# Optimization experiments

Hardware: AMD Instinct MI355X
Metric: run time of the kernel (lower is better)

## Reference

```python
import jax, jax.numpy as jnp
import numpy as np

D = 4096
N_HEAD = 32
KV_HEAD = 8
GS = D * KV_HEAD // N_HEAD  # 1024, kv projection width
B, S = 1, 2048


def setup_inputs() -> dict:
    key = jax.random.key(0)
    ks = jax.random.split(key, 10)
    sc = 0.02
    return {
        "x": jax.random.normal(ks[0], (B, S, D), dtype=jnp.float32),
        "y": jax.random.normal(ks[1], (B, S, D), dtype=jnp.float32),
        "Wq": jax.random.normal(ks[2], (D, D), dtype=jnp.float32) * sc,
        "bq": jax.random.normal(ks[3], (D,), dtype=jnp.float32) * sc,
        "Wk": jax.random.normal(ks[4], (D, GS), dtype=jnp.float32) * sc,
        "bk": jax.random.normal(ks[5], (GS,), dtype=jnp.float32) * sc,
        "Wv": jax.random.normal(ks[6], (D, GS), dtype=jnp.float32) * sc,
        "bv": jax.random.normal(ks[7], (GS,), dtype=jnp.float32) * sc,
        "Wo": jax.random.normal(ks[8], (D, D), dtype=jnp.float32) * sc,
        "bo": jax.random.normal(ks[9], (D,), dtype=jnp.float32) * sc,
        "n_head": N_HEAD,
        "kv_head": KV_HEAD,
    }


def reference(x, y, Wq, bq, Wk, bk, Wv, bv, Wo, bo, n_head, kv_head):
    b, s, d = x.shape
    hd = d // n_head              # per-head dim
    gvs = hd // 2                 # complex pairs per head (group_vector_size)
    q = (x @ Wq + bq).reshape(b, s, n_head, hd)
    k = (y @ Wk + bk).reshape(b, s, kv_head, hd)
    v = (y @ Wv + bv).reshape(b, s, kv_head, hd)

    # RoPE: phi = 1/5000**(i/gvs); angle[p, i] = phi[i] * p  (matrix.T in torch)
    phi = 1.0 / (5000.0 ** (jnp.arange(gvs, dtype=jnp.float32) / gvs))
    ang = jnp.arange(s, dtype=jnp.float32)[:, None] * phi[None, :]  # [S, gvs]
    cos = jnp.cos(ang)[None, :, None, :]  # [1,S,1,gvs]
    sin = jnp.sin(ang)[None, :, None, :]

    def rope(t):
        # interleaved pairs (t[...,2i], t[...,2i+1]) form complex numbers
        tr, ti = t[..., 0::2], t[..., 1::2]
        ro = tr * cos - ti * sin
        io = tr * sin + ti * cos
        return jnp.stack([ro, io], axis=-1).reshape(t.shape)

    q = rope(q)
    k = rope(k)

    # GQA: head h uses kv head h // (n_head // kv_head) -> repeat kv heads
    module = n_head // kv_head
    k = jnp.repeat(k, module, axis=2)  # [B,S,H,hd]
    v = jnp.repeat(v, module, axis=2)

    scores = jnp.einsum("bqhd,bkhd->bhqk", q, k) / jnp.sqrt(jnp.float32(hd))
    causal = jnp.tril(jnp.ones((s, s), dtype=bool))
    scores = jnp.where(causal[None, None], scores, -jnp.inf)
    attn = jax.nn.softmax(scores, axis=-1)
    out = jnp.einsum("bhqk,bkhd->bqhd", attn, v).reshape(b, s, d)
    return out @ Wo + bo
```

## Files before the change

### kernel.cpp

```cpp
#include <hip/hip_runtime.h>
#include <hip/hip_bf16.h>

typedef unsigned int uint32;
typedef unsigned short ushort16;
typedef __attribute__((ext_vector_type(8))) __bf16 bf16x8;
typedef __attribute__((ext_vector_type(4))) float f32x4;

__device__ __forceinline__ ushort16 f2bf(float f) {
    uint32 u = __float_as_uint(f);
    u += 0x7fff + ((u >> 16) & 1);
    return (ushort16)(u >> 16);
}
__device__ __forceinline__ uint32 pack2rn(float a, float b) {
    uint32 ua = __float_as_uint(a) + 0x8000u;
    uint32 ub = __float_as_uint(b) + 0x8000u;
    return __builtin_amdgcn_perm(ub, ua, 0x07060302);
}
__device__ __forceinline__ float blo(uint32 u) { return __uint_as_float(u << 16); }
__device__ __forceinline__ float bhi(uint32 u) { return __uint_as_float(u & 0xffff0000u); }

__device__ __forceinline__ void storeC(float v, float* p) { *p = v; }
__device__ __forceinline__ void storeC(float v, ushort16* p) { *p = f2bf(v); }

template <typename OutT>
__global__ __launch_bounds__(256) void gemm_mfma(
    const float* __restrict__ A, const float* __restrict__ W1,
    const float* __restrict__ W2, int ldw,
    const float* __restrict__ b1, const float* __restrict__ b2,
    OutT* __restrict__ C, int N, int K, int nsplit)
{
    __shared__ ushort16 As[128 * 64];
    __shared__ ushort16 Bs[128 * 64];

    const int tid  = threadIdx.x;
    const int lane = tid & 63, wave = tid >> 6;
    const int quad = lane >> 4, m16 = lane & 15;
    const int wm = (wave >> 1) * 64, wn = (wave & 1) * 64;
    const int gm0 = blockIdx.y * 128, gn0 = blockIdx.x * 128;

    const float* Wuse = (gn0 < nsplit) ? W1 : W2;
    const int ncol0 = (gn0 < nsplit) ? gn0 : gn0 - nsplit;

    f32x4 acc[4][4];
#pragma unroll
    for (int i = 0; i < 4; ++i)
#pragma unroll
        for (int j = 0; j < 4; ++j) acc[i][j] = (f32x4){0.f, 0.f, 0.f, 0.f};

    const int ra = tid >> 3, cla = tid & 7;
    const int kpb = tid >> 5, nlb = tid & 31;
    const float* Ap = A + (size_t)(gm0 + ra) * K + cla * 8;
    const float* Wp = Wuse + (size_t)(2 * kpb) * ldw + ncol0 + nlb;

    for (int k0 = 0; k0 < K; k0 += 64) {
        float4 av0[4], av1[4];
        float bv0[4][4], bv1[4][4];
#pragma unroll
        for (int t = 0; t < 4; ++t) {
            const float* ap = Ap + k0 + (size_t)(32 * t) * K;
            av0[t] = *(const float4*)ap;
            av1[t] = *(const float4*)(ap + 4);
            const float* wp = Wp + (size_t)(k0 + 16 * t) * ldw;
#pragma unroll
            for (int j = 0; j < 4; ++j) {
                bv0[t][j] = wp[32 * j];
                bv1[t][j] = wp[(size_t)ldw + 32 * j];
            }
        }
        __syncthreads();
#pragma unroll
        for (int t = 0; t < 4; ++t) {
            int r = ra + 32 * t;
            uint4 st;
            st.x = pack2rn(av0[t].x, av0[t].y);
            st.y = pack2rn(av0[t].z, av0[t].w);
            st.z = pack2rn(av1[t].x, av1[t].y);
            st.w = pack2rn(av1[t].z, av1[t].w);
            *(uint4*)&As[r * 64 + ((cla ^ (r & 7)) * 8)] = st;

            int kp = kpb + 8 * t;
            int clb = kp >> 2, kq = kp & 3;
#pragma unroll
            for (int j = 0; j < 4; ++j) {
                int n = nlb + 32 * j;
                *(uint32*)&Bs[n * 64 + (clb ^ (n & 7)) * 8 + kq * 2] =
                    pack2rn(bv0[t][j], bv1[t][j]);
            }
        }
        __syncthreads();

#pragma unroll
        for (int s = 0; s < 2; ++s) {
            bf16x8 aF[4], bF[4];
            const int cl = s * 4 + quad;
#pragma unroll
            for (int i = 0; i < 4; ++i) {
                int r = wm + i * 16 + m16;
                aF[i] = *(const bf16x8*)&As[r * 64 + (cl ^ (r & 7)) * 8];
                int n = wn + i * 16 + m16;
                bF[i] = *(const bf16x8*)&Bs[n * 64 + (cl ^ (n & 7)) * 8];
            }
#pragma unroll
            for (int i = 0; i < 4; ++i)
#pragma unroll
                for (int j = 0; j < 4; ++j)
                    acc[i][j] = __builtin_amdgcn_mfma_f32_16x16x32_bf16(
                        aF[i], bF[j], acc[i][j], 0, 0, 0);
        }
    }

#pragma unroll
    for (int j = 0; j < 4; ++j) {
        int col = gn0 + wn + j * 16 + m16;
        float bb = (col < nsplit) ? b1[col] : b2[col - nsplit];
#pragma unroll
        for (int i = 0; i < 4; ++i) {
            int row0 = gm0 + wm + i * 16 + quad * 4;
#pragma unroll
            for (int r = 0; r < 4; ++r)
                storeC(acc[i][j][r] + bb, C + (size_t)(row0 + r) * N + col);
        }
    }
}

__global__ void rope_q_kernel(float* __restrict__ T, int S)
{
    int idx = blockIdx.x * blockDim.x + threadIdx.x;
    if (idx >= S * 32 * 64) return;
    int i   = idx & 63;
    int rem = idx >> 6;
    int s   = rem >> 5;
    float inv = powf(5000.0f, -(float)i / 64.0f);
    float ang = (float)s * inv;
    float cs = cosf(ang), sn = sinf(ang);
    size_t base = (size_t)rem * 128 + 2 * i;
    float tr = T[base], ti = T[base + 1];
    T[base]     = tr * cs - ti * sn;
    T[base + 1] = tr * sn + ti * cs;
}

__global__ void rope_k_kernel(ushort16* __restrict__ KVb, int S)
{
    int idx = blockIdx.x * blockDim.x + threadIdx.x;
    if (idx >= S * 8 * 64) return;
    int i   = idx & 63;
    int rem = idx >> 6;
    int s   = rem >> 3, h = rem & 7;
    float inv = powf(5000.0f, -(float)i / 64.0f);
    float ang = (float)s * inv;
    float cs = cosf(ang), sn = sinf(ang);
    uint32* p = (uint32*)&KVb[(size_t)s * 2048 + h * 128 + 2 * i];
    uint32 u = *p;
    float tr = blo(u), ti = bhi(u);
    *p = pack2rn(tr * cs - ti * sn, tr * sn + ti * cs);
}

__global__ __launch_bounds__(256) void flash_attn_kernel(
    const float* __restrict__ Q, const ushort16* __restrict__ KVb,
    float* __restrict__ O)
{
    __shared__ __align__(16) ushort16 Ks[64 * 128];
    __shared__ __align__(16) ushort16 Vt[128 * 64];
    __shared__ __align__(16) ushort16 Ps[64 * 64];

    const int tid  = threadIdx.x;
    const int lane = tid & 63, wave = tid >> 6;
    const int quad = lane >> 4, m16 = lane & 15;
    const int h = (int)blockIdx.y, kvh = h >> 2;
    const float scale = 0.08838834764831845f * 1.4426950408889634f;

    const ushort16* Kbase = KVb + kvh * 128;
    const ushort16* Vbase = KVb + 1024 + kvh * 128;

    for (int pass = 0; pass < 2; ++pass) {
        const int qi = pass ? (int)blockIdx.x : 31 - (int)blockIdx.x;
        const int q0 = qi * 64;

        bf16x8 qa[4];
        {
            const float* qp = Q + (size_t)(q0 + wave * 16 + m16) * 4096 + h * 128 + quad * 8;
#pragma unroll
            for (int ks = 0; ks < 4; ++ks) {
                float4 a = *(const float4*)(qp + ks * 32);
                float4 b = *(const float4*)(qp + ks * 32 + 4);
                uint4 u;
                u.x = pack2rn(a.x * scale, a.y * scale);
                u.y = pack2rn(a.z * scale, a.w * scale);
                u.z = pack2rn(b.x * scale, b.y * scale);
                u.w = pack2rn(b.z * scale, b.w * scale);
                qa[ks] = *(bf16x8*)&u;
            }
        }

        f32x4 acc_o[8];
#pragma unroll
        for (int t = 0; t < 8; ++t) acc_o[t] = (f32x4){0.f, 0.f, 0.f, 0.f};
        float m_i[4], l_i[4];
#pragma unroll
        for (int r = 0; r < 4; ++r) { m_i[r] = -1e30f; l_i[r] = 0.f; }

        for (int k0 = 0; k0 <= q0; k0 += 64) {
            __syncthreads();

#pragma unroll
            for (int it = 0; it < 4; ++it) {
                int idx = tid + it * 256;
                int row = idx >> 4, c = idx & 15;
                *(uint4*)&Ks[row * 128 + ((c ^ (row & 7)) * 8)] =
                    *(const uint4*)(Kbase + (size_t)(k0 + row) * 2048 + c * 8);
            }
#pragma unroll
            for (int it = 0; it < 2; ++it) {
                int idx = tid + it * 256;
                int rp  = idx & 31;
                int dcb = (idx >> 5) * 8;
                const ushort16* p0 = Vbase + (size_t)(k0 + 2 * rp) * 2048 + dcb;
                uint4 a = *(const uint4*)p0;
                uint4 b = *(const uint4*)(p0 + 2048);
                uint32 aw[4] = {a.x, a.y, a.z, a.w}, bw[4] = {b.x, b.y, b.z, b.w};
                int cc = rp >> 2, cbase = 2 * (rp & 3);
#pragma unroll
                for (int t = 0; t < 4; ++t) {
                    int d0 = dcb + 2 * t, d1 = d0 + 1;
                    *(uint32*)&Vt[d0 * 64 + ((cc ^ (d0 & 7)) * 8) + cbase] =
                        __builtin_amdgcn_perm(bw[t], aw[t], 0x05040100);
                    *(uint32*)&Vt[d1 * 64 + ((cc ^ (d1 & 7)) * 8) + cbase] =
                        __builtin_amdgcn_perm(bw[t], aw[t], 0x07060302);
                }
            }
            __syncthreads();

            f32x4 sacc[4];
#pragma unroll
            for (int j = 0; j < 4; ++j) sacc[j] = (f32x4){0.f, 0.f, 0.f, 0.f};
            __builtin_amdgcn_s_setprio(1);
#pragma unroll
            for (int ks = 0; ks < 4; ++ks) {
#pragma unroll
                for (int j = 0; j < 4; ++j) {
                    int n = j * 16 + m16;
                    bf16x8 kb = *(const bf16x8*)&Ks[n * 128 + (((ks * 4 + quad) ^ (n & 7)) * 8)];
                    sacc[j] = __builtin_amdgcn_mfma_f32_16x16x32_bf16(qa[ks], kb, sacc[j], 0, 0, 0);
                }
            }
            __builtin_amdgcn_s_setprio(0);

            if (k0 == q0) {
                int qr = wave * 16 + quad * 4;
#pragma unroll
                for (int j = 0; j < 4; ++j) {
                    int kvl = j * 16 + m16;
#pragma unroll
                    for (int r = 0; r < 4; ++r)
                        if (kvl > qr + r) sacc[j][r] = -1e30f;
                }
            }

#pragma unroll
            for (int r = 0; r < 4; ++r) {
                float rm = fmaxf(fmaxf(sacc[0][r], sacc[1][r]), fmaxf(sacc[2][r], sacc[3][r]));
                rm = fmaxf(rm, __shfl_xor(rm, 1));
                rm = fmaxf(rm, __shfl_xor(rm, 2));
                rm = fmaxf(rm, __shfl_xor(rm, 4));
                rm = fmaxf(rm, __shfl_xor(rm, 8));
                float mnew = fmaxf(m_i[r], rm);
                float al = exp2f(m_i[r] - mnew);
                float rs = 0.f;
#pragma unroll
                for (int j = 0; j < 4; ++j) {
                    float pv = exp2f(sacc[j][r] - mnew);
                    sacc[j][r] = pv;
                    rs += pv;
                }
                rs += __shfl_xor(rs, 1);
                rs += __shfl_xor(rs, 2);
                rs += __shfl_xor(rs, 4);
                rs += __shfl_xor(rs, 8);
                l_i[r] = l_i[r] * al + rs;
                m_i[r] = mnew;
                int q = wave * 16 + quad * 4 + r;
#pragma unroll
                for (int j = 0; j < 4; ++j) {
                    int kv = j * 16 + m16;
                    Ps[q * 64 + (((kv >> 3) ^ (q & 7)) * 8) + (kv & 7)] = f2bf(sacc[j][r]);
                }
#pragma unroll
                for (int t = 0; t < 8; ++t) acc_o[t][r] *= al;
            }

            int qrow = wave * 16 + m16;
#pragma unroll
            for (int ks2 = 0; ks2 < 2; ++ks2) {
                bf16x8 pa = *(const bf16x8*)&Ps[qrow * 64 + (((ks2 * 4 + quad) ^ (qrow & 7)) * 8)];
                __builtin_amdgcn_s_setprio(1);
#pragma unroll
                for (int t = 0; t < 8; ++t) {
                    int d = t * 16 + m16;
                    bf16x8 vb = *(const bf16x8*)&Vt[d * 64 + (((ks2 * 4 + quad) ^ (d & 7)) * 8)];
                    acc_o[t] = __builtin_amdgcn_mfma_f32_16x16x32_bf16(pa, vb, acc_o[t], 0, 0, 0);
                }
                __builtin_amdgcn_s_setprio(0);
            }
        }

        float* op = O + (size_t)(q0 + wave * 16 + quad * 4) * 4096 + h * 128 + m16;
#pragma unroll
        for (int r = 0; r < 4; ++r) {
            float inv = 1.0f / l_i[r];
#pragma unroll
            for (int t = 0; t < 8; ++t)
                op[(size_t)r * 4096 + t * 16] = acc_o[t][r] * inv;
        }
    }
}

extern "C" void kernel_launch(void* const* d_in, const int* in_sizes, int n_in,
                              void* d_out, int out_size, void* d_ws, size_t ws_size,
                              hipStream_t stream)
{
    const float* x  = (const float*)d_in[0];
    const float* y  = (const float*)d_in[1];
    const float* Wq = (const float*)d_in[2];
    const float* bq = (const float*)d_in[3];
    const float* Wk = (const float*)d_in[4];
    const float* bk = (const float*)d_in[5];
    const float* Wv = (const float*)d_in[6];
    const float* bv = (const float*)d_in[7];
    const float* Wo = (const float*)d_in[8];
    const float* bo = (const float*)d_in[9];
    float* out = (float*)d_out;

    const int S = 2048, D = 4096;

    float* Q = out;
    char* ws = (char*)d_ws;
    float*    Ao  = (float*)ws;
    ushort16* KVb = (ushort16*)(ws + 34ull * 1024 * 1024);

    gemm_mfma<float><<<dim3(32, 16), 256, 0, stream>>>(
        x, Wq, Wq, D, bq, bq, Q, D, D, D);
    gemm_mfma<ushort16><<<dim3(16, 16), 256, 0, stream>>>(
        y, Wk, Wv, 1024, bk, bv, KVb, 2048, D, 1024);

    rope_q_kernel<<<(S * 32 * 64 + 255) / 256, 256, 0, stream>>>(Q, S);
    rope_k_kernel<<<(S * 8 * 64 + 255) / 256, 256, 0, stream>>>(KVb, S);

    flash_attn_kernel<<<dim3(16, 32), 256, 0, stream>>>(Q, KVb, Ao);

    gemm_mfma<float><<<dim3(32, 16), 256, 0, stream>>>(
        Ao, Wo, Wo, D, bo, bo, out, D, D, D);
}
```

Before: 681.4 us.

## Pre-convert activations and transposed weights to bf16, stage GEMM tiles via direct LDS loads

Adds pre-pass kernels that convert x and y to bf16 and transpose plus convert the weight matrices to bf16 [N,K] layout. The GEMM then loads tiles straight into LDS with global_load_lds, with no in-kernel fp32 loads, packing or strided weight reads. RoPE now writes scaled bf16 Q and attention writes bf16 output, which halves intermediate traffic for the Wo GEMM. The trade-off is extra conversion kernels launched on every call, which re-read and rewrite about 150 MB of weights and activations.

```diff
diff --git a/kernel.cpp b/kernel.cpp
--- a/kernel.cpp
+++ b/kernel.cpp
@@ -22,15 +22,54 @@
 __device__ __forceinline__ void storeC(float v, float* p) { *p = v; }
 __device__ __forceinline__ void storeC(float v, ushort16* p) { *p = f2bf(v); }
 
+__device__ __forceinline__ void gload_lds16(const void* g, void* l) {
+    __builtin_amdgcn_global_load_lds(
+        (const __attribute__((address_space(1))) unsigned int*)g,
+        (__attribute__((address_space(3))) unsigned int*)l, 16, 0, 0);
+}
+
+__global__ __launch_bounds__(256) void conv_bf16(
+    const float* __restrict__ X, ushort16* __restrict__ Xb, int n8)
+{
+    int idx = blockIdx.x * blockDim.x + threadIdx.x;
+    if (idx >= n8) return;
+    float4 a = ((const float4*)X)[2 * idx];
+    float4 b = ((const float4*)X)[2 * idx + 1];
+    uint4 u;
+    u.x = pack2rn(a.x, a.y); u.y = pack2rn(a.z, a.w);
+    u.z = pack2rn(b.x, b.y); u.w = pack2rn(b.z, b.w);
+    ((uint4*)Xb)[idx] = u;
+}
+
+__global__ __launch_bounds__(256) void transpose_w_bf16(
+    const float* __restrict__ W, ushort16* __restrict__ Wt, int N)
+{
+    __shared__ float tile[64][65];
+    const int k0 = blockIdx.x * 64, n0 = blockIdx.y * 64;
+#pragma unroll
+    for (int it = 0; it < 16; ++it) {
+        int idx = threadIdx.x + it * 256;
+        int r = idx >> 6, c = idx & 63;
+        tile[r][c] = W[(size_t)(k0 + r) * N + n0 + c];
+    }
+    __syncthreads();
+#pragma unroll
+    for (int it = 0; it < 8; ++it) {
+        int idx = threadIdx.x + it * 256;
+        int nr = idx >> 5, kp = idx & 31;
+        uint32 u = pack2rn(tile[2 * kp][nr], tile[2 * kp + 1][nr]);
+        *(uint32*)&Wt[(size_t)(n0 + nr) * 4096 + k0 + 2 * kp] = u;
+    }
+}
+
 template <typename OutT>
 __global__ __launch_bounds__(256) void gemm_mfma(
-    const float* __restrict__ A, const float* __restrict__ W1,
-    const float* __restrict__ W2, int ldw,
+    const ushort16* __restrict__ A, const ushort16* __restrict__ B,
     const float* __restrict__ b1, const float* __restrict__ b2,
     OutT* __restrict__ C, int N, int K, int nsplit)
 {
-    __shared__ ushort16 As[128 * 64];
-    __shared__ ushort16 Bs[128 * 64];
+    __shared__ __align__(16) ushort16 As[128 * 64];
+    __shared__ __align__(16) ushort16 Bs[128 * 64];
 
     const int tid  = threadIdx.x;
     const int lane = tid & 63, wave = tid >> 6;
@@ -38,74 +77,48 @@
     const int wm = (wave >> 1) * 64, wn = (wave & 1) * 64;
     const int gm0 = blockIdx.y * 128, gn0 = blockIdx.x * 128;
 
-    const float* Wuse = (gn0 < nsplit) ? W1 : W2;
-    const int ncol0 = (gn0 < nsplit) ? gn0 : gn0 - nsplit;
-
     f32x4 acc[4][4];
 #pragma unroll
     for (int i = 0; i < 4; ++i)
 #pragma unroll
         for (int j = 0; j < 4; ++j) acc[i][j] = (f32x4){0.f, 0.f, 0.f, 0.f};
 
-    const int ra = tid >> 3, cla = tid & 7;
-    const int kpb = tid >> 5, nlb = tid & 31;
-    const float* Ap = A + (size_t)(gm0 + ra) * K + cla * 8;
-    const float* Wp = Wuse + (size_t)(2 * kpb) * ldw + ncol0 + nlb;
+    const int rl = lane >> 3, cl = lane & 7;
+    const int clog = cl ^ (rl & 7);
+    const ushort16* Ag = A + (size_t)(gm0 + wave * 32 + rl) * K + clog * 8;
+    const ushort16* Bg = B + (size_t)(gn0 + wave * 32 + rl) * K + clog * 8;
+    char* AsW = (char*)As + wave * 4096;
+    char* BsW = (char*)Bs + wave * 4096;
 
     for (int k0 = 0; k0 < K; k0 += 64) {
-        float4 av0[4], av1[4];
-        float bv0[4][4], bv1[4][4];
-#pragma unroll
-        for (int t = 0; t < 4; ++t) {
-            const float* ap = Ap + k0 + (size_t)(32 * t) * K;
-            av0[t] = *(const float4*)ap;
-            av1[t] = *(const float4*)(ap + 4);
-            const float* wp = Wp + (size_t)(k0 + 16 * t) * ldw;
-#pragma unroll
-            for (int j = 0; j < 4; ++j) {
-                bv0[t][j] = wp[32 * j];
-                bv1[t][j] = wp[(size_t)ldw + 32 * j];
-            }
-        }
         __syncthreads();
 #pragma unroll
-        for (int t = 0; t < 4; ++t) {
-            int r = ra + 32 * t;
-            uint4 st;
-            st.x = pack2rn(av0[t].x, av0[t].y);
-            st.y = pack2rn(av0[t].z, av0[t].w);
-            st.z = pack2rn(av1[t].x, av1[t].y);
-            st.w = pack2rn(av1[t].z, av1[t].w);
-            *(uint4*)&As[r * 64 + ((cla ^ (r & 7)) * 8)] = st;
-
-            int kp = kpb + 8 * t;
-            int clb = kp >> 2, kq = kp & 3;
-#pragma unroll
-            for (int j = 0; j < 4; ++j) {
-                int n = nlb + 32 * j;
-                *(uint32*)&Bs[n * 64 + (clb ^ (n & 7)) * 8 + kq * 2] =
-                    pack2rn(bv0[t][j], bv1[t][j]);
-            }
-        }
+        for (int i = 0; i < 4; ++i) {
+            gload_lds16(Ag + (size_t)(8 * i) * K, AsW + i * 1024);
+            gload_lds16(Bg + (size_t)(8 * i) * K, BsW + i * 1024);
+        }
+        Ag += 64; Bg += 64;
         __syncthreads();
 
 #pragma unroll
         for (int s = 0; s < 2; ++s) {
             bf16x8 aF[4], bF[4];
-            const int cl = s * 4 + quad;
+            const int cr = s * 4 + quad;
 #pragma unroll
             for (int i = 0; i < 4; ++i) {
                 int r = wm + i * 16 + m16;
-                aF[i] = *(const bf16x8*)&As[r * 64 + (cl ^ (r & 7)) * 8];
+                aF[i] = *(const bf16x8*)&As[r * 64 + ((cr ^ (r & 7)) * 8)];
                 int n = wn + i * 16 + m16;
-                bF[i] = *(const bf16x8*)&Bs[n * 64 + (cl ^ (n & 7)) * 8];
-            }
+                bF[i] = *(const bf16x8*)&Bs[n * 64 + ((cr ^ (n & 7)) * 8)];
+            }
+            __builtin_amdgcn_s_setprio(1);
 #pragma unroll
             for (int i = 0; i < 4; ++i)
 #pragma unroll
                 for (int j = 0; j < 4; ++j)
                     acc[i][j] = __builtin_amdgcn_mfma_f32_16x16x32_bf16(
                         aF[i], bF[j], acc[i][j], 0, 0, 0);
+            __builtin_amdgcn_s_setprio(0);
         }
     }
 
@@ -123,7 +136,8 @@
     }
 }
 
-__global__ void rope_q_kernel(float* __restrict__ T, int S)
+__global__ void rope_q_kernel(const float* __restrict__ T,
+                              ushort16* __restrict__ Qb, int S)
 {
     int idx = blockIdx.x * blockDim.x + threadIdx.x;
     if (idx >= S * 32 * 64) return;
@@ -133,10 +147,11 @@
     float inv = powf(5000.0f, -(float)i / 64.0f);
     float ang = (float)s * inv;
     float cs = cosf(ang), sn = sinf(ang);
+    const float sc = 0.08838834764831845f * 1.4426950408889634f;
     size_t base = (size_t)rem * 128 + 2 * i;
     float tr = T[base], ti = T[base + 1];
-    T[base]     = tr * cs - ti * sn;
-    T[base + 1] = tr * sn + ti * cs;
+    *(uint32*)&Qb[base] = pack2rn((tr * cs - ti * sn) * sc,
+                                  (tr * sn + ti * cs) * sc);
 }
 
 __global__ void rope_k_kernel(ushort16* __restrict__ KVb, int S)
@@ -156,8 +171,8 @@
 }
 
 __global__ __launch_bounds__(256) void flash_attn_kernel(
-    const float* __restrict__ Q, const ushort16* __restrict__ KVb,
-    float* __restrict__ O)
+    const ushort16* __restrict__ Qb, const ushort16* __restrict__ KVb,
+    ushort16* __restrict__ O)
 {
     __shared__ __align__(16) ushort16 Ks[64 * 128];
     __shared__ __align__(16) ushort16 Vt[128 * 64];
@@ -167,7 +182,6 @@
     const int lane = tid & 63, wave = tid >> 6;
     const int quad = lane >> 4, m16 = lane & 15;
     const int h = (int)blockIdx.y, kvh = h >> 2;
-    const float scale = 0.08838834764831845f * 1.4426950408889634f;
 
     const ushort16* Kbase = KVb + kvh * 128;
     const ushort16* Vbase = KVb + 1024 + kvh * 128;
@@ -178,18 +192,11 @@
 
         bf16x8 qa[4];
         {
-            const float* qp = Q + (size_t)(q0 + wave * 16 + m16) * 4096 + h * 128 + quad * 8;
-#pragma unroll
-            for (int ks = 0; ks < 4; ++ks) {
-                float4 a = *(const float4*)(qp + ks * 32);
-                float4 b = *(const float4*)(qp + ks * 32 + 4);
-                uint4 u;
-                u.x = pack2rn(a.x * scale, a.y * scale);
-                u.y = pack2rn(a.z * scale, a.w * scale);
-                u.z = pack2rn(b.x * scale, b.y * scale);
-                u.w = pack2rn(b.z * scale, b.w * scale);
-                qa[ks] = *(bf16x8*)&u;
-            }
+            const ushort16* qp = Qb + (size_t)(q0 + wave * 16 + m16) * 4096
+                               + h * 128 + quad * 8;
+#pragma unroll
+            for (int ks = 0; ks < 4; ++ks)
+                qa[ks] = *(const bf16x8*)(qp + ks * 32);
         }
 
         f32x4 acc_o[8];
@@ -303,13 +310,13 @@
             }
         }
 
-        float* op = O + (size_t)(q0 + wave * 16 + quad * 4) * 4096 + h * 128 + m16;
+        ushort16* op = O + (size_t)(q0 + wave * 16 + quad * 4) * 4096 + h * 128 + m16;
 #pragma unroll
         for (int r = 0; r < 4; ++r) {
             float inv = 1.0f / l_i[r];
 #pragma unroll
             for (int t = 0; t < 8; ++t)
-                op[(size_t)r * 4096 + t * 16] = acc_o[t][r] * inv;
+                op[(size_t)r * 4096 + t * 16] = f2bf(acc_o[t][r] * inv);
         }
     }
 }
@@ -331,22 +338,37 @@
     float* out = (float*)d_out;
 
     const int S = 2048, D = 4096;
-
-    float* Q = out;
+    const size_t MB = 1024 * 1024;
+
     char* ws = (char*)d_ws;
-    float*    Ao  = (float*)ws;
-    ushort16* KVb = (ushort16*)(ws + 34ull * 1024 * 1024);
+    ushort16* xb   = (ushort16*)(ws);
+    ushort16* yb   = (ushort16*)(ws + 16 * MB);
+    ushort16* Wqt  = (ushort16*)(ws + 32 * MB);
+    ushort16* Wkvt = (ushort16*)(ws + 64 * MB);
+    ushort16* Wot  = (ushort16*)(ws + 80 * MB);
+    ushort16* KVb  = (ushort16*)(ws + 112 * MB);
+    ushort16* Qb   = xb;
+    ushort16* Ao   = yb;
+    float*    Q    = out;
+
+    const int n8 = S * D / 8;
+    conv_bf16<<<n8 / 256, 256, 0, stream>>>(x, xb, n8);
+    conv_bf16<<<n8 / 256, 256, 0, stream>>>(y, yb, n8);
+    transpose_w_bf16<<<dim3(64, 64), 256, 0, stream>>>(Wq, Wqt, D);
+    transpose_w_bf16<<<dim3(64, 16), 256, 0, stream>>>(Wk, Wkvt, 1024);
+    transpose_w_bf16<<<dim3(64, 16), 256, 0, stream>>>(Wv, Wkvt + (size_t)1024 * 4096, 1024);
+    transpose_w_bf16<<<dim3(64, 64), 256, 0, stream>>>(Wo, Wot, D);
 
     gemm_mfma<float><<<dim3(32, 16), 256, 0, stream>>>(
-        x, Wq, Wq, D, bq, bq, Q, D, D, D);
+        xb, Wqt, bq, bq, Q, D, D, D);
     gemm_mfma<ushort16><<<dim3(16, 16), 256, 0, stream>>>(
-        y, Wk, Wv, 1024, bk, bv, KVb, 2048, D, 1024);
-
-    rope_q_kernel<<<(S * 32 * 64 + 255) / 256, 256, 0, stream>>>(Q, S);
+        yb, Wkvt, bk, bv, KVb, 2048, D, 1024);
+
+    rope_q_kernel<<<(S * 32 * 64 + 255) / 256, 256, 0, stream>>>(Q, Qb, S);
     rope_k_kernel<<<(S * 8 * 64 + 255) / 256, 256, 0, stream>>>(KVb, S);
 
-    flash_attn_kernel<<<dim3(16, 32), 256, 0, stream>>>(Q, KVb, Ao);
+    flash_attn_kernel<<<dim3(16, 32), 256, 0, stream>>>(Qb, KVb, Ao);
 
     gemm_mfma<float><<<dim3(32, 16), 256, 0, stream>>>(
-        Ao, Wo, Wo, D, bo, bo, out, D, D, D);
-}
+        Ao, Wot, bo, bo, out, D, D, D);
+}
```

After: 664.9 us. 1.02x faster.
